# Kernel optimization log

Hardware: AMD Instinct MI355X
Metric: run time of the kernel (lower is better)

Reference implementation:

```python
import jax, jax.numpy as jnp
import numpy as np

N = 16384  # number of voxels


def setup_inputs() -> dict:
    key = jax.random.key(0)
    k1, k2 = jax.random.split(key)
    predictions = jax.random.normal(k1, (N,), dtype=jnp.float32)
    targets = jax.random.normal(k2, (N,), dtype=jnp.float32)
    return {"predictions": predictions, "targets": targets}


def reference(predictions, targets):
    # For each pair (i, j):  (pred_i - pred_j) - (tgt_i - tgt_j) = e_i - e_j
    # where e = predictions - targets. The original averages (e_i - e_j)^2
    # over the n*(n-1)/2 unordered pairs (i < j).
    # The full n x n matrix of (e_i - e_j)^2 is symmetric with zero diagonal,
    # so its total sum equals 2 * sum_{i<j}(e_i - e_j)^2. Dividing by
    # n*(n-1) = 2 * n_pairs gives exactly the same mean.
    n = predictions.shape[0]
    e = predictions - targets                      # [n]
    d2 = jnp.square(e[:, None] - e[None, :])       # [n, n] pairwise squared diffs
    n_f = jnp.asarray(n, d2.dtype)
    loss = d2.sum() / (n_f * (n_f - 1.0))
    return loss
```

## Files before the change

kernel.cpp:

```cpp
#include <hip/hip_runtime.h>


#define RDL_BLOCK 1024
#define RDL_N     16384
#define RDL_NVEC  (RDL_N / 4)
#define RDL_VPT   (RDL_NVEC / RDL_BLOCK)

__global__ __launch_bounds__(RDL_BLOCK)
void RelativeDifferenceLoss_kernel(const float* __restrict__ pred,
                                   const float* __restrict__ tgt,
                                   float* __restrict__ out, int n) {
    const float4* __restrict__ p4 = reinterpret_cast<const float4*>(pred);
    const float4* __restrict__ t4 = reinterpret_cast<const float4*>(tgt);
    const int tid = threadIdx.x;

    float s1 = 0.f, s2 = 0.f;

    if (n == RDL_N) {
        float4 p[RDL_VPT], t[RDL_VPT];
        #pragma unroll
        for (int k = 0; k < RDL_VPT; ++k) p[k] = p4[tid + k * RDL_BLOCK];
        #pragma unroll
        for (int k = 0; k < RDL_VPT; ++k) t[k] = t4[tid + k * RDL_BLOCK];
        #pragma unroll
        for (int k = 0; k < RDL_VPT; ++k) {
            float e0 = p[k].x - t[k].x;
            float e1 = p[k].y - t[k].y;
            float e2 = p[k].z - t[k].z;
            float e3 = p[k].w - t[k].w;
            s1 += (e0 + e1) + (e2 + e3);
            s2 += (e0 * e0 + e1 * e1) + (e2 * e2 + e3 * e3);
        }
    } else {
        const int nvec = n >> 2;
        for (int i = tid; i < nvec; i += RDL_BLOCK) {
            float4 p = p4[i];
            float4 t = t4[i];
            float e0 = p.x - t.x;
            float e1 = p.y - t.y;
            float e2 = p.z - t.z;
            float e3 = p.w - t.w;
            s1 += (e0 + e1) + (e2 + e3);
            s2 += (e0 * e0 + e1 * e1) + (e2 * e2 + e3 * e3);
        }
    }

    #pragma unroll
    for (int off = 32; off > 0; off >>= 1) {
        s1 += __shfl_down(s1, off, 64);
        s2 += __shfl_down(s2, off, 64);
    }

    __shared__ float ls1[RDL_BLOCK / 64];
    __shared__ float ls2[RDL_BLOCK / 64];
    const int wave = tid >> 6;
    const int lane = tid & 63;
    if (lane == 0) { ls1[wave] = s1; ls2[wave] = s2; }
    __syncthreads();

    if (tid == 0) {
        double S1 = 0.0, S2 = 0.0;
        #pragma unroll
        for (int w = 0; w < RDL_BLOCK / 64; ++w) {
            S1 += (double)ls1[w];
            S2 += (double)ls2[w];
        }
        const double nf = (double)n;
        const double loss = (2.0 * nf * S2 - 2.0 * S1 * S1) / (nf * (nf - 1.0));
        out[0] = (float)loss;
    }
}

extern "C" void kernel_launch(void* const* d_in, const int* in_sizes, int n_in,
                              void* d_out, int out_size, void* d_ws, size_t ws_size,
                              hipStream_t stream) {
    const float* pred = (const float*)d_in[0];
    const float* tgt  = (const float*)d_in[1];
    float* out = (float*)d_out;
    const int n = in_sizes[0];

    RelativeDifferenceLoss_kernel<<<1, RDL_BLOCK, 0, stream>>>(pred, tgt, out, n);
}
```

Baseline: 55.57 us.

## Split reduction into multi-block partial sums plus a final reduce kernel

```diff
diff --git a/kernel.cpp b/kernel.cpp
--- a/kernel.cpp
+++ b/kernel.cpp
@@ -1,47 +1,36 @@
 #include <hip/hip_runtime.h>
 
 
-#define RDL_BLOCK 1024
-#define RDL_N     16384
-#define RDL_NVEC  (RDL_N / 4)
-#define RDL_VPT   (RDL_NVEC / RDL_BLOCK)
+#define RDL_NB 64
+#define RDL_NT 64
 
-__global__ __launch_bounds__(RDL_BLOCK)
-void RelativeDifferenceLoss_kernel(const float* __restrict__ pred,
-                                   const float* __restrict__ tgt,
-                                   float* __restrict__ out, int n) {
+__global__ __launch_bounds__(RDL_NT)
+void RDL_partial(const float* __restrict__ pred,
+                 const float* __restrict__ tgt,
+                 float2* __restrict__ ws, int n) {
     const float4* __restrict__ p4 = reinterpret_cast<const float4*>(pred);
     const float4* __restrict__ t4 = reinterpret_cast<const float4*>(tgt);
-    const int tid = threadIdx.x;
+    const int nvec = n >> 2;
 
     float s1 = 0.f, s2 = 0.f;
 
-    if (n == RDL_N) {
-        float4 p[RDL_VPT], t[RDL_VPT];
-        #pragma unroll
-        for (int k = 0; k < RDL_VPT; ++k) p[k] = p4[tid + k * RDL_BLOCK];
-        #pragma unroll
-        for (int k = 0; k < RDL_VPT; ++k) t[k] = t4[tid + k * RDL_BLOCK];
-        #pragma unroll
-        for (int k = 0; k < RDL_VPT; ++k) {
-            float e0 = p[k].x - t[k].x;
-            float e1 = p[k].y - t[k].y;
-            float e2 = p[k].z - t[k].z;
-            float e3 = p[k].w - t[k].w;
-            s1 += (e0 + e1) + (e2 + e3);
-            s2 += (e0 * e0 + e1 * e1) + (e2 * e2 + e3 * e3);
-        }
-    } else {
-        const int nvec = n >> 2;
-        for (int i = tid; i < nvec; i += RDL_BLOCK) {
-            float4 p = p4[i];
-            float4 t = t4[i];
-            float e0 = p.x - t.x;
-            float e1 = p.y - t.y;
-            float e2 = p.z - t.z;
-            float e3 = p.w - t.w;
-            s1 += (e0 + e1) + (e2 + e3);
-            s2 += (e0 * e0 + e1 * e1) + (e2 * e2 + e3 * e3);
+    for (int i = blockIdx.x * RDL_NT + threadIdx.x; i < nvec;
+         i += gridDim.x * RDL_NT) {
+        float4 p = p4[i];
+        float4 t = t4[i];
+        float e0 = p.x - t.x;
+        float e1 = p.y - t.y;
+        float e2 = p.z - t.z;
+        float e3 = p.w - t.w;
+        s1 += (e0 + e1) + (e2 + e3);
+        s2 += (e0 * e0 + e1 * e1) + (e2 * e2 + e3 * e3);
+    }
+
+    if (blockIdx.x == 0) {
+        for (int i = (nvec << 2) + threadIdx.x; i < n; i += RDL_NT) {
+            float e = pred[i] - tgt[i];
+            s1 += e;
+            s2 += e * e;
         }
     }
 
@@ -51,22 +40,26 @@
         s2 += __shfl_down(s2, off, 64);
     }
 
-    __shared__ float ls1[RDL_BLOCK / 64];
-    __shared__ float ls2[RDL_BLOCK / 64];
-    const int wave = tid >> 6;
-    const int lane = tid & 63;
-    if (lane == 0) { ls1[wave] = s1; ls2[wave] = s2; }
-    __syncthreads();
+    if (threadIdx.x == 0) ws[blockIdx.x] = make_float2(s1, s2);
+}
 
-    if (tid == 0) {
-        double S1 = 0.0, S2 = 0.0;
-        #pragma unroll
-        for (int w = 0; w < RDL_BLOCK / 64; ++w) {
-            S1 += (double)ls1[w];
-            S2 += (double)ls2[w];
-        }
+__global__ __launch_bounds__(RDL_NT)
+void RDL_final(const float2* __restrict__ ws, float* __restrict__ out,
+               int n, int nb) {
+    double s1 = 0.0, s2 = 0.0;
+    for (int i = threadIdx.x; i < nb; i += RDL_NT) {
+        float2 v = ws[i];
+        s1 += (double)v.x;
+        s2 += (double)v.y;
+    }
+    #pragma unroll
+    for (int off = 32; off > 0; off >>= 1) {
+        s1 += __shfl_down(s1, off, 64);
+        s2 += __shfl_down(s2, off, 64);
+    }
+    if (threadIdx.x == 0) {
         const double nf = (double)n;
-        const double loss = (2.0 * nf * S2 - 2.0 * S1 * S1) / (nf * (nf - 1.0));
+        const double loss = (2.0 * nf * s2 - 2.0 * s1 * s1) / (nf * (nf - 1.0));
         out[0] = (float)loss;
     }
 }
@@ -77,7 +70,9 @@
     const float* pred = (const float*)d_in[0];
     const float* tgt  = (const float*)d_in[1];
     float* out = (float*)d_out;
+    float2* ws = (float2*)d_ws;
     const int n = in_sizes[0];
 
-    RelativeDifferenceLoss_kernel<<<1, RDL_BLOCK, 0, stream>>>(pred, tgt, out, n);
+    RDL_partial<<<RDL_NB, RDL_NT, 0, stream>>>(pred, tgt, ws, n);
+    RDL_final<<<1, RDL_NT, 0, stream>>>(ws, out, n, RDL_NB);
 }
```

New measurement: 56.17 us. Within noise of the previous version (+1.1%).
